# Kernel optimization log

Hardware: AMD Instinct MI355X
Metric: run time of the kernel (lower is better)

Reference implementation:

```python
import jax, jax.numpy as jnp
from jax import lax
import numpy as np

B, T, E, H, ENC, V = 64, 49, 512, 512, 1024, 32000


def setup_inputs() -> dict:
    key = jax.random.key(0)
    ks = jax.random.split(key, 12)
    embeddings = jax.random.normal(ks[0], (B, T, E), jnp.float32)
    encoder_out = jax.random.normal(ks[1], (B, ENC), jnp.float32)
    # caption lengths sorted descending (module assumes this for ragged truncation)
    lens = jax.random.randint(ks[2], (B,), 10, T + 2)
    caption_lengths = jnp.sort(lens)[::-1]
    caption_lengths = caption_lengths.at[0].set(T + 1)  # max decode length == T
    s = 1.0 / np.sqrt(H)
    u = lambda k, shp, lim: jax.random.uniform(k, shp, jnp.float32, -lim, lim)
    W_ih = u(ks[3], (4 * H, E), s)
    W_hh = u(ks[4], (4 * H, H), s)
    b_ih = u(ks[5], (4 * H,), s)
    b_hh = u(ks[6], (4 * H,), s)
    se = 1.0 / np.sqrt(ENC)
    W_init_h = u(ks[7], (H, ENC), se)
    b_init_h = u(ks[8], (H,), se)
    W_init_c = u(ks[9], (H, ENC), se)
    b_init_c = u(ks[10], (H,), se)
    W_fc = u(ks[11], (V, H), 0.1)  # init_weights: uniform(-0.1, 0.1)
    b_fc = jnp.zeros((V,), jnp.float32)
    return dict(embeddings=embeddings, encoder_out=encoder_out,
                caption_lengths=caption_lengths,
                W_ih=W_ih, W_hh=W_hh, b_ih=b_ih, b_hh=b_hh,
                W_init_h=W_init_h, b_init_h=b_init_h,
                W_init_c=W_init_c, b_init_c=b_init_c,
                W_fc=W_fc, b_fc=b_fc)


def reference(embeddings, encoder_out, caption_lengths,
              W_ih, W_hh, b_ih, b_hh,
              W_init_h, b_init_h, W_init_c, b_init_c,
              W_fc, b_fc):
    # dropout is treated as identity (eval mode) for the deterministic reference
    h0 = encoder_out @ W_init_h.T + b_init_h  # [B, H]
    c0 = encoder_out @ W_init_c.T + b_init_c
    decode_lengths = caption_lengths - 1
    Tn = embeddings.shape[1]
    # mask[t, b] = True iff example b is still active at step t
    mask = jnp.arange(Tn)[:, None] < decode_lengths[None, :]  # [T, B]
    xs = jnp.transpose(embeddings, (1, 0, 2))  # [T, B, E]

    def step(carry, inp):
        h, c = carry
        x, m = inp
        gates = x @ W_ih.T + b_ih + h @ W_hh.T + b_hh  # [B, 4H]
        i, f, g, o = jnp.split(gates, 4, axis=-1)
        i = jax.nn.sigmoid(i); f = jax.nn.sigmoid(f)
        g = jnp.tanh(g); o = jax.nn.sigmoid(o)
        c_new = f * c + i * g
        h_new = o * jnp.tanh(c_new)
        preds = h_new @ W_fc.T + b_fc  # [B, V]
        m2 = m[:, None]
        # inactive rows: state frozen (torch only updates h[:batch_size_t]),
        # predictions stay zero
        h = jnp.where(m2, h_new, h)
        c = jnp.where(m2, c_new, c)
        preds = jnp.where(m2, preds, 0.0)
        return (h, c), preds

    (_, _), preds = lax.scan(step, (h0, c0), (xs, mask))
    predictions = jnp.transpose(preds, (1, 0, 2))  # [B, T, V]
    return predictions, decode_lengths
```

## Files before the change

### kernel.cpp

```cpp
#include <hip/hip_runtime.h>
#include <stdint.h>

#define B_    64
#define T_    49
#define E_    512
#define H_    512
#define ENC_  1024
#define V_    32000
#define G4_   2048
#define M_    3136
#define MPAD_ 3200
#define NPROD 32
#define NWG   512
#define NTN   250

typedef __attribute__((ext_vector_type(8))) short bf16x8;
typedef __attribute__((ext_vector_type(4))) float f32x4;

static __device__ __forceinline__ unsigned short f2bf(float f) {
  union { float f; uint32_t u; } v; v.f = f;
  uint32_t r = v.u + 0x7FFFu + ((v.u >> 16) & 1u);
  return (unsigned short)(r >> 16);
}

static __device__ __forceinline__ void async16(const void* g, void* lds) {
  __builtin_amdgcn_global_load_lds(
      (const __attribute__((address_space(1))) unsigned int*)g,
      (__attribute__((address_space(3))) unsigned int*)lds, 16, 0, 0);
}

static __device__ __forceinline__ float sigf(float x) { return 1.0f / (1.0f + expf(-x)); }

__global__ __launch_bounds__(256) void convert_kernel(
    const float* __restrict__ Wih, const float* __restrict__ Whh,
    const float* __restrict__ emb,
    unsigned short* __restrict__ WihB, unsigned short* __restrict__ WhhB,
    unsigned short* __restrict__ AxB) {
  const int n_wih = (G4_ * E_) / 4;
  const int n_whh = (G4_ * H_) / 4;
  const int n_emb = (B_ * T_ * E_) / 4;
  const int n_pad = ((MPAD_ - M_) * E_) / 4;
  const long total = (long)n_wih + n_whh + n_emb + n_pad;
  for (long u = (long)blockIdx.x * blockDim.x + threadIdx.x; u < total;
       u += (long)gridDim.x * blockDim.x) {
    long i = u;
    if (i < n_wih) {
      float4 v = ((const float4*)Wih)[i];
      ushort4 o; o.x = f2bf(v.x); o.y = f2bf(v.y); o.z = f2bf(v.z); o.w = f2bf(v.w);
      ((ushort4*)WihB)[i] = o; continue;
    }
    i -= n_wih;
    if (i < n_whh) {
      float4 v = ((const float4*)Whh)[i];
      ushort4 o; o.x = f2bf(v.x); o.y = f2bf(v.y); o.z = f2bf(v.z); o.w = f2bf(v.w);
      ((ushort4*)WhhB)[i] = o; continue;
    }
    i -= n_whh;
    if (i < n_emb) {
      int bt = (int)(i >> 7);
      int e4 = (int)(i & 127);
      int b = bt / T_, t = bt - b * T_;
      float4 v = ((const float4*)emb)[i];
      ushort4 o; o.x = f2bf(v.x); o.y = f2bf(v.y); o.z = f2bf(v.z); o.w = f2bf(v.w);
      ((ushort4*)AxB)[((long)(t * 64 + b) << 7) + e4] = o; continue;
    }
    i -= n_emb;
    ushort4 z; z.x = z.y = z.z = z.w = 0;
    ((ushort4*)AxB)[((long)M_ << 7) + i] = z;
  }
}

__global__ __launch_bounds__(256) void init_kernel(
    const float* __restrict__ enc, const int* __restrict__ cap,
    const float* __restrict__ Wh, const float* __restrict__ bh,
    const float* __restrict__ Wc, const float* __restrict__ bc,
    unsigned short* __restrict__ h0b, float* __restrict__ c0,
    float* __restrict__ out_dl, int* __restrict__ meta,
    int* __restrict__ rowmap, int* __restrict__ zrowmap) {
  __shared__ __align__(16) float e[ENC_];
  __shared__ int s_nb[T_];
  __shared__ int s_start[T_ + 1];
  const int b = blockIdx.x, q = blockIdx.y, tid = threadIdx.x;
  ((float4*)e)[tid] = ((const float4*)(enc + (size_t)b * ENC_))[tid];
  __syncthreads();
  const bool is_c = tid >= 128;
  const int j = q * 128 + (tid & 127);
  const float* W = is_c ? Wc : Wh;
  float s = is_c ? bc[j] : bh[j];
  const float4* wr = (const float4*)(W + (size_t)j * ENC_);
  const float4* e4 = (const float4*)e;
#pragma unroll 4
  for (int k = 0; k < ENC_ / 4; ++k) {
    float4 w = wr[k], v = e4[k];
    s += w.x * v.x + w.y * v.y + w.z * v.z + w.w * v.w;
  }
  if (is_c) c0[(size_t)b * H_ + j] = s;
  else      h0b[(size_t)b * H_ + j] = f2bf(s);
  if (b == 0 && q == 0 && tid < B_) out_dl[tid] = (float)(cap[tid] - 1);

  if (b == 0 && q == 0) {
    __syncthreads();
    if (tid < T_) {
      int cnt = 0;
      for (int bb = 0; bb < B_; ++bb) cnt += (cap[bb] - 1 > tid) ? 1 : 0;
      s_nb[tid] = cnt;
    }
    __syncthreads();
    if (tid == 0) {
      int acc = 0;
      for (int t = 0; t < T_; ++t) { s_start[t] = acc; acc += s_nb[t]; }
      s_start[T_] = acc;
      const int Mc = acc;
      const int MT = (Mc + 127) >> 7;
      meta[100] = Mc;
      meta[101] = MT;
      meta[104] = M_ - Mc;
      meta[105] = NTN + (M_ - Mc) + MT * NTN;
      for (int i = Mc; i < MT * 128; ++i) rowmap[i] = -1;
    }
    __syncthreads();
    if (tid < T_) {
      meta[tid] = s_start[tid];
      const int st = s_start[tid], nb = s_nb[tid];
      for (int bb = 0; bb < nb; ++bb) rowmap[st + bb] = bb * T_ + tid;
      int zst = 0;
      for (int t2 = 0; t2 < tid; ++t2) zst += B_ - s_nb[t2];
      for (int bb = nb; bb < B_; ++bb) zrowmap[zst + (bb - nb)] = bb * T_ + tid;
    }
    __syncthreads();
    if (tid < 26) {
      const int Mc = s_start[T_];
      const int MT = (Mc + 127) >> 7;
      if (tid < MT) {
        int last = tid * 128 + 127;
        if (last > Mc - 1) last = Mc - 1;
        int tlast = 0;
        for (int t2 = 0; t2 < T_; ++t2) if (s_start[t2] <= last) tlast = t2;
        meta[110 + tid] = tlast + 1;
      }
    }
  }
}

__global__ __launch_bounds__(256) void pad_kernel(const int* __restrict__ meta,
                                                  unsigned short* __restrict__ Hall) {
  const int Mc = meta[100], MT = meta[101];
  const int tot = (MT * 128 - Mc) * 64;
  for (int i = blockIdx.x * blockDim.x + threadIdx.x; i < tot;
       i += gridDim.x * blockDim.x) {
    const int row = Mc + (i >> 6), c = i & 63;
    ushort4 z; z.x = z.y = z.z = z.w = 0;
    *(ushort4*)((char*)Hall + (size_t)row * 1024 + c * 16) = z;
  }
}

__global__ __launch_bounds__(256) void gemm_gx(
    const unsigned short* __restrict__ A, const unsigned short* __restrict__ Bm,
    float* __restrict__ C, const float* __restrict__ bias0, const float* __restrict__ bias1) {
  __shared__ __align__(16) char smem[65536];
  const int tid = threadIdx.x, lane = tid & 63, wid = tid >> 6;
  const int nt = blockIdx.x, mt = blockIdx.y;
  const int wr = wid >> 1, wc = wid & 1;
  const int m0 = mt * 128, n0 = nt * 128;
  f32x4 acc[4][4] = {};

  auto stage = [&](int buf, int kit) {
    const int k0b = kit * 128;
#pragma unroll
    for (int i = 0; i < 4; ++i) {
      int chunk = wid * 4 + i;
      int d = chunk * 1024 + lane * 16;
      int row = d >> 7, colb = d & 127;
      int sc = colb ^ ((row & 7) << 4);
      async16((const char*)A + (size_t)(m0 + row) * 1024 + k0b + sc,
              smem + buf * 16384 + chunk * 1024);
      async16((const char*)Bm + (size_t)(n0 + row) * 1024 + k0b + sc,
              smem + 32768 + buf * 16384 + chunk * 1024);
    }
  };

  stage(0, 0);
  __syncthreads();
  for (int kit = 0; kit < 8; ++kit) {
    const int buf = kit & 1;
    if (kit < 7) stage(buf ^ 1, kit + 1);
    const char* Ab = smem + buf * 16384;
    const char* Bb = smem + 32768 + buf * 16384;
#pragma unroll
    for (int kb = 0; kb < 2; ++kb) {
      const int colb = kb * 64 + (lane >> 4) * 16;
      bf16x8 af[4], bfb[4];
#pragma unroll
      for (int rt = 0; rt < 4; ++rt) {
        int ar = wr * 64 + rt * 16 + (lane & 15);
        af[rt] = *(const bf16x8*)(Ab + ar * 128 + (colb ^ ((ar & 7) << 4)));
        int br = wc * 64 + rt * 16 + (lane & 15);
        bfb[rt] = *(const bf16x8*)(Bb + br * 128 + (colb ^ ((br & 7) << 4)));
      }
#pragma unroll
      for (int i = 0; i < 4; ++i)
#pragma unroll
        for (int j = 0; j < 4; ++j)
          acc[i][j] = __builtin_amdgcn_mfma_f32_16x16x32_bf16(af[i], bfb[j], acc[i][j], 0, 0, 0);
    }
    __syncthreads();
  }
#pragma unroll
  for (int i = 0; i < 4; ++i) {
    const int rbase = m0 + wr * 64 + i * 16 + (lane >> 4) * 4;
#pragma unroll
    for (int j = 0; j < 4; ++j) {
      const int col = n0 + wc * 64 + j * 16 + (lane & 15);
#pragma unroll
      for (int r = 0; r < 4; ++r)
        C[(size_t)(rbase + r) * G4_ + col] = acc[i][j][r] + bias0[col] + bias1[col];
    }
  }
}

__global__ __launch_bounds__(256) void fused_kernel(
    const float* __restrict__ Gx, const unsigned short* __restrict__ WhhB,
    const unsigned short* __restrict__ h0b, const float* __restrict__ c0,
    unsigned short* __restrict__ hsl, unsigned short* __restrict__ Hall,
    const float* __restrict__ Wfc, unsigned short* __restrict__ WfcB,
    const float* __restrict__ bfc, const int* __restrict__ cap,
    float* __restrict__ outp, int* __restrict__ ctrl, const int* __restrict__ meta,
    const int* __restrict__ rowmap, const int* __restrict__ zrowmap) {
  __shared__ __align__(16) char smem[65536];
  const int tid = threadIdx.x, lane = tid & 63, g = tid >> 6;
  int* s_tile = (int*)(smem + 65532);

  if (blockIdx.x < NPROD) {
    __builtin_amdgcn_s_setprio(1);
    const int w = blockIdx.x, hc0 = w * 16;
    const int gcol = g * 512 + hc0 + (lane & 15);
    const int ko = (lane >> 4) * 8;
    bf16x8 wf[16];
#pragma unroll
    for (int kb = 0; kb < 16; ++kb)
      wf[kb] = *(const bf16x8*)&WhhB[(size_t)gcol * 512 + kb * 32 + ko];
    const int b = tid >> 2, hq = (tid & 3) * 4, hc = hc0 + hq;
    const int dl = cap[b] - 1;
    f32x4 creg = *(const f32x4*)&c0[b * H_ + hc];
    ushort4 hold = *(const ushort4*)&h0b[b * H_ + hc];
    const int myoff = ((b * 32) ^ (((b >> 2) & 7) << 4) ^ ((hq >> 3) << 4)) + ((hq & 7) * 2);
    {
      union { ushort4 s; unsigned long long u; } cv; cv.s = hold;
      __hip_atomic_store((unsigned long long*)((char*)hsl + w * 2048 + myoff), cv.u,
                         __ATOMIC_RELAXED, __HIP_MEMORY_SCOPE_AGENT);
    }
    int arb[4];
#pragma unroll
    for (int rt = 0; rt < 4; ++rt) {
      int ar = rt * 16 + (lane & 15);
      arb[rt] = (ar * 32) ^ (((ar >> 2) & 7) << 4) ^ (((lane >> 4) & 1) << 4);
    }
    const int chunk_hi = lane >> 5;
    float (*gl)[64][16] = (float (*)[64][16])smem;
    asm volatile("s_waitcnt vmcnt(0)" ::: "memory");
    __syncthreads();
    if (tid == 0)
      __hip_atomic_store(&ctrl[w * 16], 1, __ATOMIC_RELAXED, __HIP_MEMORY_SCOPE_AGENT);

    for (int t = 0; t < T_; ++t) {
      const size_t gxr = ((size_t)t * 64 + b) * (size_t)G4_ + hc;
      f32x4 xi = *(const f32x4*)&Gx[gxr + 0];
      f32x4 xf = *(const f32x4*)&Gx[gxr + 512];
      f32x4 xg = *(const f32x4*)&Gx[gxr + 1024];
      f32x4 xo = *(const f32x4*)&Gx[gxr + 1536];
      __builtin_amdgcn_sched_barrier(0);
      if (tid < 64) {
        const int need = t + 1;
        for (;;) {
          int v = (lane < NPROD)
                      ? __hip_atomic_load(&ctrl[lane * 16], __ATOMIC_RELAXED, __HIP_MEMORY_SCOPE_AGENT)
                      : need;
          if (__all(v >= need)) break;
          __builtin_amdgcn_s_sleep(1);
        }
        if (tid == 0 && w == 0 && t > 0)
          __hip_atomic_store(&ctrl[512], t, __ATOMIC_RELAXED, __HIP_MEMORY_SCOPE_AGENT);
      }
      __syncthreads();
      {
        const char* src = (const char*)hsl + (t & 1) * 65536 + g * 16384 + lane * 8;
        char* dst = smem + g * 16384 + lane * 8;
        unsigned long long hv[32];
#pragma unroll
        for (int i = 0; i < 32; ++i)
          hv[i] = __hip_atomic_load((const unsigned long long*)(src + i * 512),
                                    __ATOMIC_RELAXED, __HIP_MEMORY_SCOPE_AGENT);
#pragma unroll
        for (int i = 0; i < 32; ++i)
          *(unsigned long long*)(dst + i * 512) = hv[i];
      }
      __syncthreads();
      f32x4 accp[4] = {};
#pragma unroll
      for (int kb = 0; kb < 16; ++kb) {
        const int cbase = (kb * 2 + chunk_hi) * 2048;
#pragma unroll
        for (int rt = 0; rt < 4; ++rt) {
          bf16x8 af = *(const bf16x8*)(smem + cbase + arb[rt]);
          accp[rt] = __builtin_amdgcn_mfma_f32_16x16x32_bf16(af, wf[kb], accp[rt], 0, 0, 0);
        }
      }
      __syncthreads();
#pragma unroll
      for (int rt = 0; rt < 4; ++rt)
#pragma unroll
        for (int r = 0; r < 4; ++r)
          gl[g][rt * 16 + (lane >> 4) * 4 + r][lane & 15] = accp[rt][r];
      __syncthreads();
      f32x4 vi = xi + *(const f32x4*)&gl[0][b][hq];
      f32x4 vf = xf + *(const f32x4*)&gl[1][b][hq];
      f32x4 vg = xg + *(const f32x4*)&gl[2][b][hq];
      f32x4 vo = xo + *(const f32x4*)&gl[3][b][hq];
      f32x4 cn;
      ushort4 hb16;
      {
        float hv[4];
#pragma unroll
        for (int k = 0; k < 4; ++k) {
          float iv = sigf(vi[k]), fv = sigf(vf[k]), gv = tanhf(vg[k]), ov = sigf(vo[k]);
          cn[k] = fv * creg[k] + iv * gv;
          hv[k] = ov * tanhf(cn[k]);
        }
        hb16.x = f2bf(hv[0]); hb16.y = f2bf(hv[1]); hb16.z = f2bf(hv[2]); hb16.w = f2bf(hv[3]);
      }
      if (t < dl) {
        union { ushort4 s; unsigned long long u; } cv; cv.s = hb16;
        __hip_atomic_store((unsigned long long*)&Hall[((size_t)(meta[t] + b)) * H_ + hc],
                           cv.u, __ATOMIC_RELAXED, __HIP_MEMORY_SCOPE_AGENT);
        hold = hb16; creg = cn;
      }
      if (t + 1 < T_) {
        union { ushort4 s; unsigned long long u; } cv; cv.s = hold;
        __hip_atomic_store(
            (unsigned long long*)((char*)hsl + ((t + 1) & 1) * 65536 + w * 2048 + myoff),
            cv.u, __ATOMIC_RELAXED, __HIP_MEMORY_SCOPE_AGENT);
      }
      asm volatile("s_waitcnt vmcnt(0)" ::: "memory");
      __syncthreads();
      if (tid == 0)
        __hip_atomic_store(&ctrl[w * 16], t + 2, __ATOMIC_RELAXED, __HIP_MEMORY_SCOPE_AGENT);
    }
    if (w == 0 && tid < 64) {
      const int need = T_ + 1;
      for (;;) {
        int v = (lane < NPROD)
                    ? __hip_atomic_load(&ctrl[lane * 16], __ATOMIC_RELAXED, __HIP_MEMORY_SCOPE_AGENT)
                    : need;
        if (__all(v >= need)) break;
        __builtin_amdgcn_s_sleep(1);
      }
      if (tid == 0)
        __hip_atomic_store(&ctrl[512], T_, __ATOMIC_RELAXED, __HIP_MEMORY_SCOPE_AGENT);
    }
    __builtin_amdgcn_s_setprio(0);
  }

  const int NZI = meta[104];
  const int NTOT = meta[105];
  const int wid = tid >> 6;
  const int wr = wid >> 1, wc = wid & 1;
  for (;;) {
    __syncthreads();
    if (tid == 0)
      *s_tile = __hip_atomic_fetch_add(&ctrl[528], 1, __ATOMIC_RELAXED, __HIP_MEMORY_SCOPE_AGENT);
    __syncthreads();
    const int tile = *s_tile;
    if (tile >= NTOT) break;

    if (tile < NTN) {
      const float4* src = (const float4*)(Wfc + (size_t)tile * 128 * 512);
      unsigned long long* dst = (unsigned long long*)WfcB + (size_t)tile * 16384;
      for (int i = tid; i < 16384; i += 256) {
        float4 v = src[i];
        union { ushort4 s; unsigned long long u; } cv;
        cv.s.x = f2bf(v.x); cv.s.y = f2bf(v.y); cv.s.z = f2bf(v.z); cv.s.w = f2bf(v.w);
        __hip_atomic_store(&dst[i], cv.u, __ATOMIC_RELAXED, __HIP_MEMORY_SCOPE_AGENT);
      }
      asm volatile("s_waitcnt vmcnt(0)" ::: "memory");
      __syncthreads();
      if (tid == 0)
        __hip_atomic_fetch_add(&ctrl[544], 1, __ATOMIC_RELAXED, __HIP_MEMORY_SCOPE_AGENT);
      continue;
    }

    if (tile < NTN + NZI) {
      const int bt = zrowmap[tile - NTN];
      f32x4* dst = (f32x4*)(outp + (size_t)bt * V_);
      f32x4 z = {0.0f, 0.0f, 0.0f, 0.0f};
      for (int i = tid; i < V_ / 4; i += 256) dst[i] = z;
      continue;
    }

    const int gt = tile - NTN - NZI;
    const int mt = gt / NTN, nt = gt - mt * NTN;
    const int m0 = mt * 128, n0 = nt * 128;
    const int need = meta[110 + mt];
    if (tid == 0) {
      while (__hip_atomic_load(&ctrl[544], __ATOMIC_RELAXED, __HIP_MEMORY_SCOPE_AGENT) < NTN)
        __builtin_amdgcn_s_sleep(2);
      while (__hip_atomic_load(&ctrl[512], __ATOMIC_RELAXED, __HIP_MEMORY_SCOPE_AGENT) < need)
        __builtin_amdgcn_s_sleep(8);
    }
    __syncthreads();

    f32x4 acc[4][4] = {};
    auto stage = [&](int buf, int kit) {
      const int k0b = kit * 128;
#pragma unroll
      for (int i = 0; i < 4; ++i) {
        int chunk = wid * 4 + i;
        int d = chunk * 1024 + lane * 16;
        int row = d >> 7, colb = d & 127;
        int sc = colb ^ ((row & 7) << 4);
        async16((const char*)Hall + (size_t)(m0 + row) * 1024 + k0b + sc,
                smem + buf * 16384 + chunk * 1024);
        async16((const char*)WfcB + (size_t)(n0 + row) * 1024 + k0b + sc,
                smem + 32768 + buf * 16384 + chunk * 1024);
      }
    };
    stage(0, 0);
    __syncthreads();
    for (int kit = 0; kit < 8; ++kit) {
      const int buf = kit & 1;
      if (kit < 7) stage(buf ^ 1, kit + 1);
      const char* Ab = smem + buf * 16384;
      const char* Bb = smem + 32768 + buf * 16384;
#pragma unroll
      for (int kb = 0; kb < 2; ++kb) {
        const int colb = kb * 64 + (lane >> 4) * 16;
        bf16x8 af[4], bfb[4];
#pragma unroll
        for (int rt = 0; rt < 4; ++rt) {
          int ar = wr * 64 + rt * 16 + (lane & 15);
          af[rt] = *(const bf16x8*)(Ab + ar * 128 + (colb ^ ((ar & 7) << 4)));
          int br = wc * 64 + rt * 16 + (lane & 15);
          bfb[rt] = *(const bf16x8*)(Bb + br * 128 + (colb ^ ((br & 7) << 4)));
        }
#pragma unroll
        for (int i = 0; i < 4; ++i)
#pragma unroll
          for (int j = 0; j < 4; ++j)
            acc[i][j] = __builtin_amdgcn_mfma_f32_16x16x32_bf16(af[i], bfb[j], acc[i][j], 0, 0, 0);
      }
      __syncthreads();
    }
    float* Ct = (float*)smem;
#pragma unroll
    for (int j = 0; j < 4; ++j) {
      const int colL = wc * 64 + j * 16 + (lane & 15);
      const float bz = bfc[n0 + colL];
#pragma unroll
      for (int i = 0; i < 4; ++i) {
        const int rb = wr * 64 + i * 16 + (lane >> 4) * 4;
#pragma unroll
        for (int r = 0; r < 4; ++r) {
          const int row = rb + r;
          Ct[row * 128 + (colL ^ ((row & 7) << 2))] = acc[i][j][r] + bz;
        }
      }
    }
    __syncthreads();
    const int c4 = tid & 31;
    const int rsub = tid >> 5;
#pragma unroll
    for (int itr = 0; itr < 16; ++itr) {
      const int row = itr * 8 + rsub;
      const int bt = rowmap[m0 + row];
      if (bt < 0) continue;
      f32x4 v = *(const f32x4*)&Ct[row * 128 + ((c4 ^ (row & 7)) << 2)];
      *(f32x4*)(outp + (size_t)bt * V_ + n0 + (c4 << 2)) = v;
    }
  }
}

extern "C" void kernel_launch(void* const* d_in, const int* in_sizes, int n_in,
                              void* d_out, int out_size, void* d_ws, size_t ws_size,
                              hipStream_t stream) {
  const float* emb = (const float*)d_in[0];
  const float* enc = (const float*)d_in[1];
  const int*   cap = (const int*)d_in[2];
  const float* Wih = (const float*)d_in[3];
  const float* Whh = (const float*)d_in[4];
  const float* bih = (const float*)d_in[5];
  const float* bhh = (const float*)d_in[6];
  const float* Wh0 = (const float*)d_in[7];
  const float* bh0 = (const float*)d_in[8];
  const float* Wc0 = (const float*)d_in[9];
  const float* bc0 = (const float*)d_in[10];
  const float* Wfc = (const float*)d_in[11];
  const float* bfc = (const float*)d_in[12];
  float* out = (float*)d_out;

  char* ws = (char*)d_ws;
  size_t o = 0;
  auto carve = [&](size_t bytes) { void* p = ws + o; o += (bytes + 255) & ~(size_t)255; return p; };
  unsigned short* WihB = (unsigned short*)carve((size_t)G4_ * E_ * 2);
  unsigned short* WhhB = (unsigned short*)carve((size_t)G4_ * H_ * 2);
  unsigned short* WfcB = (unsigned short*)carve((size_t)V_ * H_ * 2);
  unsigned short* AxB  = (unsigned short*)carve((size_t)MPAD_ * E_ * 2);
  float*          Gx   = (float*)carve((size_t)MPAD_ * G4_ * 4);
  unsigned short* Hall = (unsigned short*)carve((size_t)MPAD_ * H_ * 2);
  unsigned short* h0b  = (unsigned short*)carve((size_t)B_ * H_ * 2);
  float*          cst  = (float*)carve((size_t)B_ * H_ * 4);
  unsigned short* hsl  = (unsigned short*)carve((size_t)2 * 65536);
  int*            ctrl = (int*)carve(4096);
  int*            meta = (int*)carve(1024);
  int*            rowmap = (int*)carve((size_t)MPAD_ * 4);
  int*            zrowmap = (int*)carve((size_t)MPAD_ * 4);
  (void)ws_size; (void)in_sizes; (void)n_in; (void)out_size;

  hipMemsetAsync(ctrl, 0, 4096, stream);
  convert_kernel<<<dim3(1024), dim3(256), 0, stream>>>(Wih, Whh, emb, WihB, WhhB, AxB);
  init_kernel<<<dim3(64, 4), dim3(256), 0, stream>>>(enc, cap, Wh0, bh0, Wc0, bc0, h0b, cst,
                                                     out + (size_t)B_ * T_ * V_,
                                                     meta, rowmap, zrowmap);
  pad_kernel<<<dim3(32), dim3(256), 0, stream>>>(meta, Hall);
  gemm_gx<<<dim3(G4_ / 128, MPAD_ / 128), dim3(256), 0, stream>>>(AxB, WihB, Gx, bih, bhh);
  fused_kernel<<<dim3(NWG), dim3(256), 0, stream>>>(Gx, WhhB, h0b, cst, hsl, Hall,
                                                    Wfc, WfcB, bfc, cap, out, ctrl,
                                                    meta, rowmap, zrowmap);
}
```

Before: 399.2 us.

## Co-locate recurrent producer blocks on one XCC and use wider coherent loads

Producer roles are now assigned dynamically: each block reads its XCC id, the first XCC to gather 32 blocks claims the producer role, and those blocks take slots 0..31. Keeping all recurrent producers on a single XCC lets them share L2, so per-step h exchanges can use plain stores and sc0 dwordx4 loads instead of agent-scope atomics. The h gather is widened from 8-byte to 16-byte loads. This adds a startup rendezvous across all blocks and depends on XCC-local cache coherence for correctness.

```diff
diff --git a/kernel.cpp b/kernel.cpp
--- a/kernel.cpp
+++ b/kernel.cpp
@@ -229,10 +229,41 @@
   __shared__ __align__(16) char smem[65536];
   const int tid = threadIdx.x, lane = tid & 63, g = tid >> 6;
   int* s_tile = (int*)(smem + 65532);
-
-  if (blockIdx.x < NPROD) {
+  int* s_role = (int*)(smem + 65528);
+
+  {
+    int xcc;
+    asm volatile("s_getreg_b32 %0, hwreg(HW_REG_XCC_ID)" : "=s"(xcc));
+    if (tid == 0) {
+      xcc &= 7;
+      int a = __hip_atomic_fetch_add(&ctrl[592 + xcc * 16], 1, __ATOMIC_RELAXED,
+                                     __HIP_MEMORY_SCOPE_AGENT);
+      if (a == NPROD - 1) {
+        int expected = 0;
+        __hip_atomic_compare_exchange_strong(&ctrl[560], &expected, xcc + 1,
+                                             __ATOMIC_RELAXED, __ATOMIC_RELAXED,
+                                             __HIP_MEMORY_SCOPE_AGENT);
+      }
+      int e;
+      for (;;) {
+        e = __hip_atomic_load(&ctrl[560], __ATOMIC_RELAXED, __HIP_MEMORY_SCOPE_AGENT);
+        if (e) break;
+        __builtin_amdgcn_s_sleep(2);
+      }
+      int slot = NPROD;
+      if (e - 1 == xcc)
+        slot = __hip_atomic_fetch_add(&ctrl[576], 1, __ATOMIC_RELAXED,
+                                      __HIP_MEMORY_SCOPE_AGENT);
+      *s_role = slot;
+    }
+    __syncthreads();
+  }
+  const int w = *s_role;
+  __syncthreads();
+
+  if (w < NPROD) {
     __builtin_amdgcn_s_setprio(1);
-    const int w = blockIdx.x, hc0 = w * 16;
+    const int hc0 = w * 16;
     const int gcol = g * 512 + hc0 + (lane & 15);
     const int ko = (lane >> 4) * 8;
     bf16x8 wf[16];
@@ -246,8 +277,7 @@
     const int myoff = ((b * 32) ^ (((b >> 2) & 7) << 4) ^ ((hq >> 3) << 4)) + ((hq & 7) * 2);
     {
       union { ushort4 s; unsigned long long u; } cv; cv.s = hold;
-      __hip_atomic_store((unsigned long long*)((char*)hsl + w * 2048 + myoff), cv.u,
-                         __ATOMIC_RELAXED, __HIP_MEMORY_SCOPE_AGENT);
+      *(unsigned long long*)((char*)hsl + w * 2048 + myoff) = cv.u;
     }
     int arb[4];
 #pragma unroll
@@ -283,16 +313,17 @@
       }
       __syncthreads();
       {
-        const char* src = (const char*)hsl + (t & 1) * 65536 + g * 16384 + lane * 8;
-        char* dst = smem + g * 16384 + lane * 8;
-        unsigned long long hv[32];
-#pragma unroll
-        for (int i = 0; i < 32; ++i)
-          hv[i] = __hip_atomic_load((const unsigned long long*)(src + i * 512),
-                                    __ATOMIC_RELAXED, __HIP_MEMORY_SCOPE_AGENT);
-#pragma unroll
-        for (int i = 0; i < 32; ++i)
-          *(unsigned long long*)(dst + i * 512) = hv[i];
+        const char* src = (const char*)hsl + (t & 1) * 65536 + g * 16384 + lane * 16;
+        char* dst = smem + g * 16384 + lane * 16;
+        int4 hv[16];
+#pragma unroll
+        for (int i = 0; i < 16; ++i)
+          asm volatile("global_load_dwordx4 %0, %1, off sc0"
+                       : "=&v"(hv[i]) : "v"(src + i * 1024));
+        asm volatile("s_waitcnt vmcnt(0)" ::: "memory");
+#pragma unroll
+        for (int i = 0; i < 16; ++i)
+          *(int4*)(dst + i * 1024) = hv[i];
       }
       __syncthreads();
       f32x4 accp[4] = {};
@@ -319,14 +350,14 @@
       f32x4 cn;
       ushort4 hb16;
       {
-        float hv[4];
+        float hv4[4];
 #pragma unroll
         for (int k = 0; k < 4; ++k) {
           float iv = sigf(vi[k]), fv = sigf(vf[k]), gv = tanhf(vg[k]), ov = sigf(vo[k]);
           cn[k] = fv * creg[k] + iv * gv;
-          hv[k] = ov * tanhf(cn[k]);
+          hv4[k] = ov * tanhf(cn[k]);
         }
-        hb16.x = f2bf(hv[0]); hb16.y = f2bf(hv[1]); hb16.z = f2bf(hv[2]); hb16.w = f2bf(hv[3]);
+        hb16.x = f2bf(hv4[0]); hb16.y = f2bf(hv4[1]); hb16.z = f2bf(hv4[2]); hb16.w = f2bf(hv4[3]);
       }
       if (t < dl) {
         union { ushort4 s; unsigned long long u; } cv; cv.s = hb16;
@@ -336,9 +367,7 @@
       }
       if (t + 1 < T_) {
         union { ushort4 s; unsigned long long u; } cv; cv.s = hold;
-        __hip_atomic_store(
-            (unsigned long long*)((char*)hsl + ((t + 1) & 1) * 65536 + w * 2048 + myoff),
-            cv.u, __ATOMIC_RELAXED, __HIP_MEMORY_SCOPE_AGENT);
+        *(unsigned long long*)((char*)hsl + ((t + 1) & 1) * 65536 + w * 2048 + myoff) = cv.u;
       }
       asm volatile("s_waitcnt vmcnt(0)" ::: "memory");
       __syncthreads();
@@ -370,6 +399,7 @@
       *s_tile = __hip_atomic_fetch_add(&ctrl[528], 1, __ATOMIC_RELAXED, __HIP_MEMORY_SCOPE_AGENT);
     __syncthreads();
     const int tile = *s_tile;
+    __syncthreads();
     if (tile >= NTOT) break;
 
     if (tile < NTN) {
```

Result: no change. 397.4 us (-0.4%).
